# Kernel tuning notes

Hardware: AMD Instinct MI355X
Metric: run time of the kernel (lower is better)

Reference implementation:

```python
import jax, jax.numpy as jnp
import numpy as np

N, C, L, K = 150000, 256, 50000, 200  # nodes, classes(=feature dim), labeled count, top-k


def setup_inputs() -> dict:
    key = jax.random.key(0)
    k1, k2 = jax.random.split(key)
    inputs = jax.random.normal(k1, (N, C), dtype=jnp.float32)
    cls = jax.random.randint(k2, (N,), 0, C)
    labels = jax.nn.one_hot(cls, C, dtype=jnp.float32)  # one-hot label matrix [N, C]
    labels_mask = jnp.arange(N) < L      # first L nodes labeled
    unlabels_mask = ~labels_mask
    return {"inputs": inputs, "labels": labels, "labels_mask": labels_mask,
            "unlabels_mask": unlabels_mask, "k": K}


def _l2n(x):
    # tf.nn.l2_normalize with epsilon 1e-12
    return x * jax.lax.rsqrt(jnp.maximum(jnp.sum(x * x, axis=-1, keepdims=True), 1e-12))


def reference(inputs, labels, labels_mask, unlabels_mask, k):
    lm = labels_mask.astype(inputs.dtype)    # [N]
    um = unlabels_mask.astype(inputs.dtype)  # [N]
    # protos: per-class mean of labeled features (masked matmul == boolean_mask + matmul)
    total = jnp.einsum('nf,nc->fc', inputs * lm[:, None], labels)  # [F, C]
    weight = 1.0 / jnp.sum(labels, 0)                               # 1/count per class (over ALL labels, as in TF)
    protos = (total * weight[None, :]).T                            # [C, F]
    # cosine similarity of every node to every prototype [N, C]
    prob = _l2n(inputs) @ _l2n(protos).T
    # per-row top-k, scattered back to a sparse [N, C] (raw top values, softmax in TF was dead code)
    vals, idx = jax.lax.top_k(prob, k)                              # [N, k]
    rows = jnp.arange(prob.shape[0])[:, None]
    sparse = jnp.zeros_like(prob).at[rows, idx].set(vals)
    p = sparse * um[:, None]                                        # only unlabeled rows contribute
    # per-class normalization: denom_c = sum_u p[u,c] + n_labeled_c
    denom = jnp.sum(p, 0) + jnp.sum(labels * lm[:, None], 0)        # [C]
    w = p / denom[None, :]                                          # [N, C]
    # change[c] = sum_u w[u,c] * (x_u - protos[c])
    change = w.T @ inputs - jnp.sum(w, 0)[:, None] * protos         # [C, F]
    protos = protos + change
    logits = _l2n(inputs) @ _l2n(protos).T                          # [N, C]
    return logits
```

## Files before the change

kernel.cpp:

```cpp
#include <hip/hip_runtime.h>

typedef unsigned int uint;
typedef unsigned short ushort;
typedef float f32x4 __attribute__((ext_vector_type(4)));
typedef uint u32x4 __attribute__((ext_vector_type(4)));
typedef uint u32x2 __attribute__((ext_vector_type(2)));
typedef __bf16 bf16x8 __attribute__((ext_vector_type(8)));

constexpr int NR = 150000;
constexpr int CD = 256;
constexpr int LR = 50000;
constexpr int KEX = 56;
constexpr int NB1 = 49984;
constexpr int NUP = 100032;
constexpr int NTP = 150080;

__device__ __forceinline__ ushort f2bf(float x) {
  uint u = __builtin_bit_cast(uint, x);
  u += 0x7FFFu + ((u >> 16) & 1u);
  return (ushort)(u >> 16);
}
__device__ __forceinline__ uint key16(uint b) {
  return (b & 0x8000u) ? (~b & 0xFFFFu) : (b | 0x8000u);
}

__global__ __launch_bounds__(256) void k_cls(const float* __restrict__ labels,
                                             int* __restrict__ cls,
                                             float* __restrict__ ca,
                                             float* __restrict__ cl) {
  __shared__ int ha[256], hl[256];
  int t = threadIdx.x;
  ha[t] = 0; hl[t] = 0;
  __syncthreads();
  int lane = t & 63;
  int wid = (blockIdx.x << 2) | (t >> 6);
  int nw = gridDim.x << 2;
  for (int n = wid; n < NR; n += nw) {
    f32x4 v = *reinterpret_cast<const f32x4*>(&labels[n * CD + lane * 4]);
    int j = v[0] > 0.5f ? 0 : v[1] > 0.5f ? 1 : v[2] > 0.5f ? 2 : v[3] > 0.5f ? 3 : -1;
    if (j >= 0) {
      int c = lane * 4 + j;
      cls[n] = c;
      atomicAdd(&ha[c], 1);
      if (n < LR) atomicAdd(&hl[c], 1);
    }
  }
  __syncthreads();
  atomicAdd(&ca[t], (float)ha[t]);
  atomicAdd(&cl[t], (float)hl[t]);
}

__global__ __launch_bounds__(256) void k_prep(const float* __restrict__ X,
                                              ushort* __restrict__ Xt,
                                              float* __restrict__ invn) {
  __shared__ __align__(16) ushort xl[64 * 264];
  __shared__ float red[256];
  int t = threadIdx.x;
  int r = t >> 2, cq = t & 3;
  int g0 = blockIdx.x * 64;
  int g = g0 + r;
  bool valid = g < NR;
  float ss = 0.f;
#pragma unroll
  for (int j = 0; j < 16; ++j) {
    int col = cq * 4 + j * 16;
    f32x4 x = valid ? *reinterpret_cast<const f32x4*>(&X[g * CD + col])
                    : (f32x4){0.f, 0.f, 0.f, 0.f};
    ss += x[0] * x[0] + x[1] * x[1] + x[2] * x[2] + x[3] * x[3];
    uint p0 = (uint)f2bf(x[0]) | ((uint)f2bf(x[1]) << 16);
    uint p1 = (uint)f2bf(x[2]) | ((uint)f2bf(x[3]) << 16);
    *reinterpret_cast<u32x2*>(&xl[r * 264 + col]) = (u32x2){p0, p1};
  }
  red[t] = ss;
  __syncthreads();
  if (t < 64) {
    float s4 = red[t * 4] + red[t * 4 + 1] + red[t * 4 + 2] + red[t * 4 + 3];
    if (g0 + t < NR) invn[g0 + t] = rsqrtf(fmaxf(s4, 1e-12f));
  }
  ushort* xp = Xt + (size_t)blockIdx.x * 16384;
  int f = t;
  uint buf[4];
  for (int n = 0; n < 64; ++n) {
    ushort v16 = xl[n * 264 + f];
    int sl = n & 7;
    if (sl & 1) buf[sl >> 1] |= (uint)v16 << 16; else buf[sl >> 1] = v16;
    if (sl == 7)
      *reinterpret_cast<u32x4*>(&xp[f * 64 + n - 7]) =
          (u32x4){buf[0], buf[1], buf[2], buf[3]};
  }
}

template <int KIND>
__global__ __launch_bounds__(1024) void k_gemmB(const int* __restrict__ cls,
                                                const ushort* __restrict__ Ap,
                                                const ushort* __restrict__ Xt,
                                                float* __restrict__ P,
                                                int nch, int nbase) {
  __shared__ __align__(16) ushort Al[256 * 40];
  __shared__ __align__(16) ushort Bl[256 * 40];
  int t = threadIdx.x;
  int lane = t & 63, w = t >> 6;
  int m = lane & 15, qd = lane >> 4;
  int cR = t >> 2, off = (t & 3) * 8;
  f32x4 acc[16];
#pragma unroll
  for (int i = 0; i < 16; ++i) acc[i] = (f32x4){0.f, 0.f, 0.f, 0.f};

  if (KIND == 0) {
    for (int i = t; i < 5120; i += 1024) reinterpret_cast<uint*>(Al)[i] = 0u;
  }

  u32x4 aR, bR;
  int curc = -1, prevc = -1;
  int ch = blockIdx.x;
  if (ch < nch) {
    int n0 = ch * 32;
    if (KIND == 1) {
      const ushort* ap = Ap + (size_t)(n0 >> 6) * 16384 + (n0 & 63);
      aR = *reinterpret_cast<const u32x4*>(&ap[cR * 64 + off]);
    } else if (t < 32) {
      int gg = n0 + t;
      curc = (gg < LR) ? cls[gg] : -1;
    }
    int gr = nbase + n0;
    const ushort* xp = Xt + (size_t)(gr >> 6) * 16384 + (gr & 63);
    bR = *reinterpret_cast<const u32x4*>(&xp[cR * 64 + off]);
  }

  for (; ch < nch; ch += gridDim.x) {
    __syncthreads();
    if (KIND == 0) {
      if (t < 32) {
        if (prevc >= 0) Al[prevc * 40 + t] = 0;
        if (curc >= 0) Al[curc * 40 + t] = 0x3F80;
        prevc = curc;
      }
    } else {
      *reinterpret_cast<u32x4*>(&Al[cR * 40 + off]) = aR;
    }
    *reinterpret_cast<u32x4*>(&Bl[cR * 40 + off]) = bR;
    int chn = ch + gridDim.x;
    if (chn < nch) {
      int n0 = chn * 32;
      if (KIND == 1) {
        const ushort* ap = Ap + (size_t)(n0 >> 6) * 16384 + (n0 & 63);
        aR = *reinterpret_cast<const u32x4*>(&ap[cR * 64 + off]);
      } else if (t < 32) {
        int gg = n0 + t;
        curc = (gg < LR) ? cls[gg] : -1;
      }
      int gr = nbase + n0;
      const ushort* xp = Xt + (size_t)(gr >> 6) * 16384 + (gr & 63);
      bR = *reinterpret_cast<const u32x4*>(&xp[cR * 64 + off]);
    }
    __syncthreads();
    bf16x8 a = *reinterpret_cast<const bf16x8*>(&Al[(w * 16 + m) * 40 + qd * 8]);
#pragma unroll
    for (int ft = 0; ft < 16; ++ft) {
      bf16x8 b = *reinterpret_cast<const bf16x8*>(&Bl[(ft * 16 + m) * 40 + qd * 8]);
      acc[ft] = __builtin_amdgcn_mfma_f32_16x16x32_bf16(a, b, acc[ft], 0, 0, 0);
    }
  }
  float* Ps = P + (size_t)blockIdx.x * 65536;
#pragma unroll
  for (int ft = 0; ft < 16; ++ft)
#pragma unroll
    for (int r = 0; r < 4; ++r)
      Ps[(w * 16 + qd * 4 + r) * 256 + ft * 16 + m] = acc[ft][r];
}

__global__ __launch_bounds__(256) void k_protos(const float* __restrict__ P, int nsl,
                                                const float* __restrict__ ca,
                                                float* __restrict__ protos,
                                                ushort* __restrict__ phat) {
  __shared__ float red[256];
  int c = blockIdx.x, f = threadIdx.x;
  float s = 0.f;
  for (int i = 0; i < nsl; ++i) s += P[i * 65536 + c * 256 + f];
  float cnt = ca[c];
  float pv = cnt > 0.5f ? s / cnt : 0.f;
  protos[c * 256 + f] = pv;
  red[f] = pv * pv;
  __syncthreads();
  for (int st = 128; st > 0; st >>= 1) {
    if (f < st) red[f] += red[f + st];
    __syncthreads();
  }
  float iv = rsqrtf(fmaxf(red[0], 1e-12f));
  phat[c * 256 + f] = f2bf(pv * iv);
}

__global__ __launch_bounds__(256) void k_update(const float* __restrict__ PS, int nsl,
                                                const float* __restrict__ protos,
                                                const float* __restrict__ q,
                                                const float* __restrict__ clab,
                                                ushort* __restrict__ phat2) {
  __shared__ float red[256];
  int c = blockIdx.x, f = threadIdx.x;
  float s = 0.f;
  for (int i = 0; i < nsl; ++i) s += PS[i * 65536 + c * 256 + f];
  float qc = q[c];
  float den = qc + clab[c];
  float pv = protos[c * 256 + f];
  float np = pv + (s - qc * pv) / den;
  red[f] = np * np;
  __syncthreads();
  for (int st = 128; st > 0; st >>= 1) {
    if (f < st) red[f] += red[f + st];
    __syncthreads();
  }
  float iv = rsqrtf(fmaxf(red[0], 1e-12f));
  phat2[c * 256 + f] = f2bf(np * iv);
}

template <int TOPK>
__global__ __launch_bounds__(256, 4) void k_passA(const float* __restrict__ X,
                                                  const float* __restrict__ invn,
                                                  const ushort* __restrict__ Bm,
                                                  float* __restrict__ out,
                                                  ushort* __restrict__ pt,
                                                  float* __restrict__ q,
                                                  int gbase) {
  __shared__ __align__(16) char smem[TOPK ? 35072 : 25600];
  ushort* Al = reinterpret_cast<ushort*>(smem);
  ushort* Bl = reinterpret_cast<ushort*>(smem + 5120);
  int t = threadIdx.x;
  int lane = t & 63, w = t >> 6;
  int m = lane & 15, qd = lane >> 4;
  int g0 = gbase + blockIdx.x * 64;
  int row = t >> 2, off = (t & 3) * 8;
  int g = g0 + row;
  bool valid = g < NR;
  float inv = valid ? invn[g] : 0.f;
  f32x4 acc[16];
#pragma unroll
  for (int i = 0; i < 16; ++i) acc[i] = (f32x4){0.f, 0.f, 0.f, 0.f};

  f32x4 x0 = valid ? *reinterpret_cast<const f32x4*>(&X[g * CD + off])
                   : (f32x4){0.f, 0.f, 0.f, 0.f};
  f32x4 x1 = valid ? *reinterpret_cast<const f32x4*>(&X[g * CD + off + 4])
                   : (f32x4){0.f, 0.f, 0.f, 0.f};
  u32x4 bR[4];
#pragma unroll
  for (int i = 0; i < 4; ++i)
    bR[i] = *reinterpret_cast<const u32x4*>(&Bm[((t >> 2) + i * 64) * 256 + off]);

  for (int k0 = 0; k0 < 256; k0 += 32) {
    f32x4 y0 = x0 * inv, y1 = x1 * inv;
    uint u0 = (uint)f2bf(y0[0]) | ((uint)f2bf(y0[1]) << 16);
    uint u1 = (uint)f2bf(y0[2]) | ((uint)f2bf(y0[3]) << 16);
    uint u2 = (uint)f2bf(y1[0]) | ((uint)f2bf(y1[1]) << 16);
    uint u3 = (uint)f2bf(y1[2]) | ((uint)f2bf(y1[3]) << 16);
    __syncthreads();
    *reinterpret_cast<u32x4*>(&Al[row * 40 + off]) = (u32x4){u0, u1, u2, u3};
#pragma unroll
    for (int i = 0; i < 4; ++i)
      *reinterpret_cast<u32x4*>(&Bl[((t >> 2) + i * 64) * 40 + off]) = bR[i];
    if (k0 < 224) {
      int kn = k0 + 32;
      x0 = valid ? *reinterpret_cast<const f32x4*>(&X[g * CD + kn + off])
                 : (f32x4){0.f, 0.f, 0.f, 0.f};
      x1 = valid ? *reinterpret_cast<const f32x4*>(&X[g * CD + kn + off + 4])
                 : (f32x4){0.f, 0.f, 0.f, 0.f};
#pragma unroll
      for (int i = 0; i < 4; ++i)
        bR[i] = *reinterpret_cast<const u32x4*>(
            &Bm[((t >> 2) + i * 64) * 256 + kn + off]);
    }
    __syncthreads();
    bf16x8 a = *reinterpret_cast<const bf16x8*>(&Al[(w * 16 + m) * 40 + qd * 8]);
#pragma unroll
    for (int ft = 0; ft < 16; ++ft) {
      bf16x8 b = *reinterpret_cast<const bf16x8*>(&Bl[(ft * 16 + m) * 40 + qd * 8]);
      acc[ft] = __builtin_amdgcn_mfma_f32_16x16x32_bf16(a, b, acc[ft], 0, 0, 0);
    }
  }

  if constexpr (TOPK == 0) {
#pragma unroll
    for (int ft = 0; ft < 16; ++ft)
#pragma unroll
      for (int r = 0; r < 4; ++r) {
        int rr = w * 16 + qd * 4 + r;
        int gg = g0 + rr;
        if (gg < NR) out[gg * 256 + ft * 16 + m] = acc[ft][r];
      }
  } else {
    ushort* s16 = reinterpret_cast<ushort*>(smem);
    uint* tkey = reinterpret_cast<uint*>(smem + 34816);
    __syncthreads();
#pragma unroll
    for (int ft = 0; ft < 16; ++ft)
#pragma unroll
      for (int r = 0; r < 4; ++r)
        s16[(w * 16 + qd * 4 + r) * 272 + ft * 16 + m] = f2bf(acc[ft][r]);
    __syncthreads();
    for (int i0 = 0; i0 < 16; i0 += 4) {
      uint kk[4][4];
      uint mth[4];
#pragma unroll
      for (int rr = 0; rr < 4; ++rr) {
        int rw = w * 16 + i0 + rr;
        u32x2 pk = *reinterpret_cast<const u32x2*>(&s16[rw * 272 + lane * 4]);
        kk[rr][0] = key16(pk[0] & 0xFFFFu);
        kk[rr][1] = key16(pk[0] >> 16);
        kk[rr][2] = key16(pk[1] & 0xFFFFu);
        kk[rr][3] = key16(pk[1] >> 16);
        mth[rr] = 0u;
      }
      for (int b = 15; b >= 0; --b) {
#pragma unroll
        for (int rr = 0; rr < 4; ++rr) {
          uint cand = mth[rr] | (1u << b);
          int cnt = __builtin_popcountll(__ballot(kk[rr][0] < cand)) +
                    __builtin_popcountll(__ballot(kk[rr][1] < cand)) +
                    __builtin_popcountll(__ballot(kk[rr][2] < cand)) +
                    __builtin_popcountll(__ballot(kk[rr][3] < cand));
          if (cnt <= KEX) mth[rr] = cand;
        }
      }
      if (lane == 0) {
#pragma unroll
        for (int rr = 0; rr < 4; ++rr) tkey[w * 16 + i0 + rr] = mth[rr];
      }
    }
    __syncthreads();
    int c = t;
    float qloc = 0.f;
    uint buf[4];
    ushort* pp = pt + (size_t)blockIdx.x * 16384;
    for (int n = 0; n < 64; ++n) {
      int grow = g0 + n;
      ushort v16 = s16[n * 272 + c];
      bool keep = (key16(v16) >= tkey[n]) && (grow >= LR) && (grow < NR);
      ushort pv16 = keep ? v16 : (ushort)0;
      if (keep) qloc += __builtin_bit_cast(float, (uint)v16 << 16);
      int sl = n & 7;
      if (sl & 1) buf[sl >> 1] |= (uint)pv16 << 16; else buf[sl >> 1] = pv16;
      if (sl == 7)
        *reinterpret_cast<u32x4*>(&pp[c * 64 + n - 7]) =
            (u32x4){buf[0], buf[1], buf[2], buf[3]};
    }
    atomicAdd(&q[c], qloc);
  }
}

extern "C" void kernel_launch(void* const* d_in, const int* in_sizes, int n_in,
                              void* d_out, int out_size, void* d_ws, size_t ws_size,
                              hipStream_t stream) {
  const float* inputs = (const float*)d_in[0];
  const float* labels = (const float*)d_in[1];
  float* out = (float*)d_out;

  ushort* p_t = (ushort*)d_out;
  ushort* Xt  = (ushort*)((char*)d_out + (size_t)256 * NUP * 2);

  char* ws = (char*)d_ws;
  float* q      = (float*)(ws + 0);
  float* c_all  = (float*)(ws + 1024);
  float* c_lab  = (float*)(ws + 2048);
  float* protos = (float*)(ws + 4096);
  ushort* phat  = (ushort*)(ws + 4096 + 262144);
  ushort* phat2 = (ushort*)(ws + 4096 + 262144 + 131072);
  float* invn   = (float*)(ws + 528384);
  int*   cls    = (int*)(ws + 1128384);
  size_t base = 1736704;
  int sT = 128, sS = 256;
  while (base + (size_t)(sT + sS) * 262144ULL > ws_size) {
    if (sS > sT) sS >>= 1; else if (sT > 8) sT >>= 1; else break;
  }
  float* PT = (float*)(ws + base);
  float* PS = PT + (size_t)sT * 65536;

  hipMemsetAsync(ws, 0, 3072, stream);

  k_cls<<<1024, 256, 0, stream>>>(labels, cls, c_all, c_lab);
  k_prep<<<NTP / 64, 256, 0, stream>>>(inputs, Xt, invn);
  k_gemmB<0><<<sT, 1024, 0, stream>>>(cls, nullptr, Xt, PT, 1563, 0);
  k_protos<<<256, 256, 0, stream>>>(PT, sT, c_all, protos, phat);
  k_passA<1><<<NUP / 64, 256, 0, stream>>>(inputs, invn, phat, nullptr, p_t, q, NB1);
  k_gemmB<1><<<sS, 1024, 0, stream>>>(nullptr, p_t, Xt, PS, NUP / 32, NB1);
  k_update<<<256, 256, 0, stream>>>(PS, sS, protos, q, c_lab, phat2);
  k_passA<0><<<(NR + 63) / 64, 256, 0, stream>>>(inputs, invn, phat2, out, nullptr, nullptr, 0);
}
```

Measured before the change: 719.4 us.

## Load MFMA operands directly from global memory, bypassing LDS staging in passA

The GEMM in k_passA no longer stages A and B tiles through shared memory. Each lane now loads its own A fragment from X, normalizes it and converts it to bf16 in registers, and reads B fragments straight from global memory, which should mostly hit cache. This removes the per-step LDS writes and the two __syncthreads barriers, and shrinks shared memory for the non-topk variant, which can raise occupancy. The trade-off is more global and cache traffic per wave with no reuse of B across the block. Separately, the class-histogram kernel unrolls its row loop by four so more loads are in flight at once.

After: 915.6 us. 1.27x slower.

```diff
diff --git a/kernel.cpp b/kernel.cpp
--- a/kernel.cpp
+++ b/kernel.cpp
@@ -35,8 +35,27 @@
   int lane = t & 63;
   int wid = (blockIdx.x << 2) | (t >> 6);
   int nw = gridDim.x << 2;
-  for (int n = wid; n < NR; n += nw) {
-    f32x4 v = *reinterpret_cast<const f32x4*>(&labels[n * CD + lane * 4]);
+  int n = wid;
+  for (; n + 3 * nw < NR; n += 4 * nw) {
+    f32x4 v[4];
+#pragma unroll
+    for (int u = 0; u < 4; ++u)
+      v[u] = *reinterpret_cast<const f32x4*>(&labels[(size_t)(n + u * nw) * CD + lane * 4]);
+#pragma unroll
+    for (int u = 0; u < 4; ++u) {
+      int nn = n + u * nw;
+      int j = v[u][0] > 0.5f ? 0 : v[u][1] > 0.5f ? 1 : v[u][2] > 0.5f ? 2
+                                                      : v[u][3] > 0.5f ? 3 : -1;
+      if (j >= 0) {
+        int c = lane * 4 + j;
+        cls[nn] = c;
+        atomicAdd(&ha[c], 1);
+        if (nn < LR) atomicAdd(&hl[c], 1);
+      }
+    }
+  }
+  for (; n < NR; n += nw) {
+    f32x4 v = *reinterpret_cast<const f32x4*>(&labels[(size_t)n * CD + lane * 4]);
     int j = v[0] > 0.5f ? 0 : v[1] > 0.5f ? 1 : v[2] > 0.5f ? 2 : v[3] > 0.5f ? 3 : -1;
     if (j >= 0) {
       int c = lane * 4 + j;
@@ -221,57 +240,39 @@
                                                   ushort* __restrict__ pt,
                                                   float* __restrict__ q,
                                                   int gbase) {
-  __shared__ __align__(16) char smem[TOPK ? 35072 : 25600];
-  ushort* Al = reinterpret_cast<ushort*>(smem);
-  ushort* Bl = reinterpret_cast<ushort*>(smem + 5120);
+  __shared__ __align__(16) char smem[TOPK ? 35072 : 16];
   int t = threadIdx.x;
   int lane = t & 63, w = t >> 6;
   int m = lane & 15, qd = lane >> 4;
   int g0 = gbase + blockIdx.x * 64;
-  int row = t >> 2, off = (t & 3) * 8;
-  int g = g0 + row;
-  bool valid = g < NR;
-  float inv = valid ? invn[g] : 0.f;
+  int g2 = g0 + w * 16 + m;
+  bool v2 = g2 < NR;
+  float inv2 = v2 ? invn[g2] : 0.f;
+  const float* xp = X + (size_t)(v2 ? g2 : 0) * CD + qd * 8;
+  const ushort* bp = Bm + m * 256 + qd * 8;
   f32x4 acc[16];
 #pragma unroll
   for (int i = 0; i < 16; ++i) acc[i] = (f32x4){0.f, 0.f, 0.f, 0.f};
 
-  f32x4 x0 = valid ? *reinterpret_cast<const f32x4*>(&X[g * CD + off])
-                   : (f32x4){0.f, 0.f, 0.f, 0.f};
-  f32x4 x1 = valid ? *reinterpret_cast<const f32x4*>(&X[g * CD + off + 4])
-                   : (f32x4){0.f, 0.f, 0.f, 0.f};
-  u32x4 bR[4];
-#pragma unroll
-  for (int i = 0; i < 4; ++i)
-    bR[i] = *reinterpret_cast<const u32x4*>(&Bm[((t >> 2) + i * 64) * 256 + off]);
+  f32x4 x0 = *reinterpret_cast<const f32x4*>(&xp[0]);
+  f32x4 x1 = *reinterpret_cast<const f32x4*>(&xp[4]);
 
   for (int k0 = 0; k0 < 256; k0 += 32) {
-    f32x4 y0 = x0 * inv, y1 = x1 * inv;
+    f32x4 y0 = x0 * inv2, y1 = x1 * inv2;
     uint u0 = (uint)f2bf(y0[0]) | ((uint)f2bf(y0[1]) << 16);
     uint u1 = (uint)f2bf(y0[2]) | ((uint)f2bf(y0[3]) << 16);
     uint u2 = (uint)f2bf(y1[0]) | ((uint)f2bf(y1[1]) << 16);
     uint u3 = (uint)f2bf(y1[2]) | ((uint)f2bf(y1[3]) << 16);
-    __syncthreads();
-    *reinterpret_cast<u32x4*>(&Al[row * 40 + off]) = (u32x4){u0, u1, u2, u3};
-#pragma unroll
-    for (int i = 0; i < 4; ++i)
-      *reinterpret_cast<u32x4*>(&Bl[((t >> 2) + i * 64) * 40 + off]) = bR[i];
+    u32x4 au = (u32x4){u0, u1, u2, u3};
+    bf16x8 a = __builtin_bit_cast(bf16x8, au);
     if (k0 < 224) {
-      int kn = k0 + 32;
-      x0 = valid ? *reinterpret_cast<const f32x4*>(&X[g * CD + kn + off])
-                 : (f32x4){0.f, 0.f, 0.f, 0.f};
-      x1 = valid ? *reinterpret_cast<const f32x4*>(&X[g * CD + kn + off + 4])
-                 : (f32x4){0.f, 0.f, 0.f, 0.f};
-#pragma unroll
-      for (int i = 0; i < 4; ++i)
-        bR[i] = *reinterpret_cast<const u32x4*>(
-            &Bm[((t >> 2) + i * 64) * 256 + kn + off]);
-    }
-    __syncthreads();
-    bf16x8 a = *reinterpret_cast<const bf16x8*>(&Al[(w * 16 + m) * 40 + qd * 8]);
+      x0 = *reinterpret_cast<const f32x4*>(&xp[k0 + 32]);
+      x1 = *reinterpret_cast<const f32x4*>(&xp[k0 + 36]);
+    }
 #pragma unroll
     for (int ft = 0; ft < 16; ++ft) {
-      bf16x8 b = *reinterpret_cast<const bf16x8*>(&Bl[(ft * 16 + m) * 40 + qd * 8]);
+      u32x4 bu = *reinterpret_cast<const u32x4*>(&bp[ft * 4096 + k0]);
+      bf16x8 b = __builtin_bit_cast(bf16x8, bu);
       acc[ft] = __builtin_amdgcn_mfma_f32_16x16x32_bf16(a, b, acc[ft], 0, 0, 0);
     }
   }
@@ -288,13 +289,11 @@
   } else {
     ushort* s16 = reinterpret_cast<ushort*>(smem);
     uint* tkey = reinterpret_cast<uint*>(smem + 34816);
-    __syncthreads();
 #pragma unroll
     for (int ft = 0; ft < 16; ++ft)
 #pragma unroll
       for (int r = 0; r < 4; ++r)
         s16[(w * 16 + qd * 4 + r) * 272 + ft * 16 + m] = f2bf(acc[ft][r]);
-    __syncthreads();
     for (int i0 = 0; i0 < 16; i0 += 4) {
       uint kk[4][4];
       uint mth[4];
```
